# Kernel tuning notes

Measured on AMD Instinct MI355X. Metric: run time of the kernel, lower is better.

Reference implementation:

```python
import jax, jax.numpy as jnp
import numpy as np

H1, H2, H3 = 128, 64, 32   # hidden sizes from source constants
NT = 2                      # n_targets (P_I_meas, Q_I_meas)
NF = 16                     # n_features
B, T, S = 4096, 200, 20     # batch, history length, OUTPUT_STEPS


def setup_inputs() -> dict:
    key = jax.random.key(0)
    ks = jax.random.split(key, 16)
    s1 = 1.0 / np.sqrt(H1)  # pytorch LSTM init scale
    s2 = 1.0 / np.sqrt(H2)
    s3 = 1.0 / np.sqrt(H3)
    f32 = jnp.float32
    return {
        "x_history": jax.random.normal(ks[0], (B, T, NF), dtype=f32),
        "x_future_refs": jax.random.normal(ks[1], (B, S, NF - NT), dtype=f32),
        "Wih1": jax.random.normal(ks[2], (4 * H1, NF), dtype=f32) * s1,
        "Whh1": jax.random.normal(ks[3], (4 * H1, H1), dtype=f32) * s1,
        "bih1": jax.random.normal(ks[4], (4 * H1,), dtype=f32) * s1,
        "bhh1": jax.random.normal(ks[5], (4 * H1,), dtype=f32) * s1,
        "Wih2": jax.random.normal(ks[6], (4 * H2, H1), dtype=f32) * s2,
        "Whh2": jax.random.normal(ks[7], (4 * H2, H2), dtype=f32) * s2,
        "bih2": jax.random.normal(ks[8], (4 * H2,), dtype=f32) * s2,
        "bhh2": jax.random.normal(ks[9], (4 * H2,), dtype=f32) * s2,
        "Wd": jax.random.normal(ks[10], (H3, H2), dtype=f32) * s2,
        "bd": jax.random.normal(ks[11], (H3,), dtype=f32) * s2,
        "Wf": jax.random.normal(ks[12], (NT, H3), dtype=f32) * s3,
        "bf": jax.random.normal(ks[13], (NT,), dtype=f32) * s3,
        "out_bias": jnp.zeros((NT,), dtype=f32),
    }


def lstm_cell(x, h, c, Wih, Whh, bih, bhh):
    # PyTorch gate order: i, f, g, o
    g = x @ Wih.T + h @ Whh.T + (bih + bhh)
    i, f, gg, o = jnp.split(g, 4, axis=-1)
    c_new = jax.nn.sigmoid(f) * c + jax.nn.sigmoid(i) * jnp.tanh(gg)
    h_new = jax.nn.sigmoid(o) * jnp.tanh(c_new)
    return h_new, c_new


def reference(x_history, x_future_refs, Wih1, Whh1, bih1, bhh1,
              Wih2, Whh2, bih2, bhh2, Wd, bd, Wf, bf, out_bias):
    b = x_history.shape[0]
    dt = x_history.dtype
    h1 = jnp.zeros((b, H1), dt); c1 = jnp.zeros((b, H1), dt)
    h2 = jnp.zeros((b, H2), dt); c2 = jnp.zeros((b, H2), dt)

    # --- encode history: stacked 2-layer LSTM over T steps ---
    def enc_step(carry, xt):
        h1, c1, h2, c2 = carry
        h1, c1 = lstm_cell(xt, h1, c1, Wih1, Whh1, bih1, bhh1)
        h2, c2 = lstm_cell(h1, h2, c2, Wih2, Whh2, bih2, bhh2)
        return (h1, c1, h2, c2), None

    (h1, c1, h2, c2), _ = jax.lax.scan(
        enc_step, (h1, c1, h2, c2), jnp.swapaxes(x_history, 0, 1))

    # last history targets: x_history[:, -1, n_non_targets:]
    cur = x_history[:, -1, NF - NT:]

    def dec_step(carry, ref):
        h1, c1, h2, c2, cur = carry
        xin = jnp.concatenate([ref, cur], axis=1)  # [B, NF]
        h1, c1 = lstm_cell(xin, h1, c1, Wih1, Whh1, bih1, bhh1)
        h2, c2 = lstm_cell(h1, h2, c2, Wih2, Whh2, bih2, bhh2)
        d = jax.nn.relu(h2 @ Wd.T + bd)
        pred = d @ Wf.T + bf + out_bias
        return (h1, c1, h2, c2, pred), pred

    _, preds = jax.lax.scan(
        dec_step, (h1, c1, h2, c2, cur), jnp.swapaxes(x_future_refs, 0, 1))
    return jnp.swapaxes(preds, 0, 1)  # [B, S, NT]
```

## Files before the change

kernel.cpp:

```cpp
#include <hip/hip_runtime.h>

typedef unsigned short u16;
typedef unsigned int u32;

using short8 = __attribute__((ext_vector_type(8))) short;
using f32x4  = __attribute__((ext_vector_type(4))) float;

#define LOG2E 1.44269504088896340736f

#define X1S 168
#define H2S 72
#define DBS 40

__device__ __forceinline__ u16 f2bf(float f) {
  u32 u = __float_as_uint(f);
  return (u16)((u + 0x7FFFu + ((u >> 16) & 1u)) >> 16);
}
__device__ __forceinline__ float sigm(float x) {
  return __builtin_amdgcn_rcpf(1.0f + __builtin_amdgcn_exp2f(-LOG2E * x));
}
__device__ __forceinline__ float tanh_(float x) {
  return 1.0f - 2.0f * __builtin_amdgcn_rcpf(1.0f + __builtin_amdgcn_exp2f(2.0f * LOG2E * x));
}
__device__ __forceinline__ f32x4 mfma_(short8 a, short8 b, f32x4 c) {
  return __builtin_amdgcn_mfma_f32_16x16x32_bf16(a, b, c, 0, 0, 0);
}

__global__ __launch_bounds__(512, 1) void spc_lstm(
    const float* __restrict__ xh,   const float* __restrict__ xfr,
    const float* __restrict__ Wih1, const float* __restrict__ Whh1,
    const float* __restrict__ bih1, const float* __restrict__ bhh1,
    const float* __restrict__ Wih2, const float* __restrict__ Whh2,
    const float* __restrict__ bih2, const float* __restrict__ bhh2,
    const float* __restrict__ Wd,   const float* __restrict__ bd,
    const float* __restrict__ Wf,   const float* __restrict__ bfv,
    const float* __restrict__ ob,   float* __restrict__ out)
{
  __shared__ __align__(16) u16 X1[2][16 * X1S];
  __shared__ __align__(16) u16 H2B[2][16 * H2S];
  __shared__ __align__(16) u16 DB[16 * DBS];
  __shared__ __align__(16) u16 W1xF[32 * 256];
  __shared__ __align__(16) u16 W2F[64 * 512];
  __shared__ __align__(16) u16 WdF[4 * 512];
  __shared__ __align__(16) u16 WfF[512];
  __shared__ u16 PREDV[16][2];

  const int tid = threadIdx.x;
  const int wv  = tid >> 6;
  const int l   = tid & 63;
  const int c   = l & 15;
  const int q   = l >> 4;
  const int bb  = blockIdx.x << 4;
  const bool isA = (wv < 4);

  short8 w1h[4][4];
  short8 w2h[4][2];
  float  b1r[4];
  float  b2r[4] = {0.f, 0.f, 0.f, 0.f};

  for (int i = tid; i < 2 * 16 * X1S; i += 512) ((u16*)X1)[i] = 0;
  for (int i = tid; i < 2 * 16 * H2S; i += 512) ((u16*)H2B)[i] = 0;
  for (int i = tid; i < 16 * DBS; i += 512) DB[i] = 0;
  if (tid < 32) ((u16*)PREDV)[tid] = 0;
  __syncthreads();

  for (int i = tid; i < 64 * 512; i += 512) {
    const int rid = i >> 9, e = i & 511, k = e >> 4, n = e & 15;
    const int ww = rid >> 4, ty = (rid >> 2) & 3, kc = rid & 3;
    const int g = ty * 64 + ww * 16 + n;
    W2F[rid * 512 + ((k >> 3) * 16 + n) * 8 + (k & 7)] = f2bf(Wih2[g * 128 + kc * 32 + k]);
  }
  for (int i = tid; i < 32 * 256; i += 512) {
    const int T = i >> 8, e = i & 255, k = e >> 4, n = e & 15;
    const int ty = T >> 3, uv = T & 7;
    const int g = ty * 128 + uv * 16 + n;
    W1xF[T * 256 + ((k >> 3) * 16 + n) * 8 + (k & 7)] = f2bf(Wih1[g * 16 + k]);
  }
  for (int i = tid; i < 4 * 512; i += 512) {
    const int tix = i >> 9, e = i & 511, k = e >> 4, n = e & 15;
    const int ww = tix >> 1, kc2 = tix & 1;
    WdF[tix * 512 + ((k >> 3) * 16 + n) * 8 + (k & 7)] =
        f2bf(Wd[(ww * 16 + n) * 64 + kc2 * 32 + k]);
  }
  {
    const int k = tid >> 4, n = tid & 15;
    if (tid < 512)
      WfF[((k >> 3) * 16 + n) * 8 + (k & 7)] = (n < 2) ? f2bf(Wf[n * 32 + k]) : (u16)0;
  }

  #pragma unroll
  for (int ty = 0; ty < 4; ty++) {
    const int g = ty * 128 + wv * 16 + c;
    b1r[ty] = bih1[g] + bhh1[g];
    #pragma unroll
    for (int kc = 0; kc < 4; kc++) {
      short8 v;
      #pragma unroll
      for (int j = 0; j < 8; j++)
        v[j] = (short)f2bf(Whh1[g * 128 + kc * 32 + q * 8 + j]);
      w1h[ty][kc] = v;
    }
  }
  if (isA) {
    #pragma unroll
    for (int ty = 0; ty < 4; ty++) {
      const int g2 = ty * 64 + wv * 16 + c;
      b2r[ty] = bih2[g2] + bhh2[g2];
      #pragma unroll
      for (int kc = 0; kc < 2; kc++) {
        short8 v;
        #pragma unroll
        for (int j = 0; j < 8; j++)
          v[j] = (short)f2bf(Whh2[g2 * 64 + kc * 32 + q * 8 + j]);
        w2h[ty][kc] = v;
      }
    }
  }
  const float bdr = (wv == 4 || wv == 5) ? bd[(wv - 4) * 16 + c] : 0.f;
  const float bfr = (wv == 4 && c < 2) ? (bfv[c] + ob[c]) : 0.f;

  const int xi = tid - 256, xr = (xi >> 4) & 15, xcc = xi & 15;
  float xreg = 0.f; bool dreg = false;
  if (!isA) {
    X1[0][xr * X1S + 128 + xcc] = f2bf(xh[(bb + xr) * 3200 + xcc]);
    xreg = xh[(bb + xr) * 3200 + 16 + xcc]; dreg = true;
  }
  f32x4 c1 = (f32x4){0,0,0,0};
  f32x4 c2 = (f32x4){0,0,0,0};
  __syncthreads();

  for (int t = 0; t <= 220; t++) {
    u16* Xc    = X1[t & 1];
    u16* Xn    = X1[(t + 1) & 1];
    u16* Hprev = H2B[t & 1];
    u16* Hdst  = H2B[(t + 1) & 1];
    const bool dec  = (t >= 201);
    const bool doL1 = (t <= 219);
    const bool doL2 = isA && (t >= 1);

    if (doL2) {
      f32x4 acc2[4];
      #pragma unroll
      for (int ty = 0; ty < 4; ty++)
        acc2[ty] = (f32x4){b2r[ty], b2r[ty], b2r[ty], b2r[ty]};
      #pragma unroll
      for (int kc = 0; kc < 4; kc++) {
        const short8 fhi = *(const short8*)&Xc[c * X1S + kc * 32 + q * 8];
        #pragma unroll
        for (int ty = 0; ty < 4; ty++) {
          const short8 wf_ = *(const short8*)&W2F[(wv * 16 + ty * 4 + kc) * 512 + l * 8];
          acc2[ty] = mfma_(fhi, wf_, acc2[ty]);
        }
      }
      #pragma unroll
      for (int kc = 0; kc < 2; kc++) {
        const short8 hhi = *(const short8*)&Hprev[c * H2S + kc * 32 + q * 8];
        #pragma unroll
        for (int ty = 0; ty < 4; ty++)
          acc2[ty] = mfma_(hhi, w2h[ty][kc], acc2[ty]);
      }
      const int u = wv * 16 + c;
      #pragma unroll
      for (int r = 0; r < 4; r++) {
        float ig = sigm(acc2[0][r]);
        float fg = sigm(acc2[1][r]);
        float gg = tanh_(acc2[2][r]);
        float og = sigm(acc2[3][r]);
        float cn = fg * c2[r] + ig * gg;
        float hn = og * tanh_(cn);
        c2[r] = cn;
        Hdst[(q * 4 + r) * H2S + u] = f2bf(hn);
      }
    }

    if (!isA) {
      const float xw = xreg; const bool dw = dreg;
      const int s2 = t + 2;
      dreg = false;
      if (s2 < 200) { xreg = xh[(bb + xr) * 3200 + s2 * 16 + xcc]; dreg = true; }
      else if (s2 < 220) {
        const int s = s2 - 200;
        if (xcc < 14)    { xreg = xfr[(bb + xr) * 280 + s * 14 + xcc]; dreg = true; }
        else if (s == 0) { xreg = xh[(bb + xr) * 3200 + 199 * 16 + xcc]; dreg = true; }
      }
      if (dw) Xn[xr * X1S + 128 + xcc] = f2bf(xw);
    }

    if (dec) {
      __syncthreads();
      if (wv == 4 || wv == 5) {
        const int ww = wv - 4;
        f32x4 accd = (f32x4){bdr, bdr, bdr, bdr};
        #pragma unroll
        for (int kc = 0; kc < 2; kc++) {
          const short8 ad  = *(const short8*)&Hdst[c * H2S + kc * 32 + q * 8];
          const short8 wdk = *(const short8*)&WdF[(ww * 2 + kc) * 512 + l * 8];
          accd = mfma_(ad, wdk, accd);
        }
        #pragma unroll
        for (int r = 0; r < 4; r++)
          DB[(q * 4 + r) * DBS + ww * 16 + c] = f2bf(fmaxf(accd[r], 0.f));
      }
      __syncthreads();
      if (wv == 4) {
        const short8 ap  = *(const short8*)&DB[c * DBS + q * 8];
        const short8 wfv = *(const short8*)&WfF[l * 8];
        f32x4 accp = (f32x4){bfr, bfr, bfr, bfr};
        accp = mfma_(ap, wfv, accp);
        if (c < 2) {
          #pragma unroll
          for (int r = 0; r < 4; r++) {
            const int b = q * 4 + r;
            out[(bb + b) * 40 + (t - 201) * 2 + c] = accp[r];
            PREDV[b][c] = f2bf(accp[r]);
          }
        }
      }
      __syncthreads();
    }

    if (doL1) {
      f32x4 acc1[4];
      #pragma unroll
      for (int ty = 0; ty < 4; ty++)
        acc1[ty] = (f32x4){b1r[ty], b1r[ty], b1r[ty], b1r[ty]};
      #pragma unroll
      for (int kc = 0; kc < 4; kc++) {
        const short8 ahi = *(const short8*)&Xc[c * X1S + kc * 32 + q * 8];
        #pragma unroll
        for (int ty = 0; ty < 4; ty++)
          acc1[ty] = mfma_(ahi, w1h[ty][kc], acc1[ty]);
      }
      {
        short8 ax = *(const short8*)&Xc[c * X1S + 128 + q * 8];
        if (dec && q == 1) {
          ax[6] = (short)PREDV[c][0];
          ax[7] = (short)PREDV[c][1];
        }
        #pragma unroll
        for (int ty = 0; ty < 4; ty++) {
          short8 wxv = (short8){0,0,0,0,0,0,0,0};
          if (q < 2)
            wxv = *(const short8*)&W1xF[(ty * 8 + wv) * 256 + l * 8];
          acc1[ty] = mfma_(ax, wxv, acc1[ty]);
        }
      }
      const int u = wv * 16 + c;
      #pragma unroll
      for (int r = 0; r < 4; r++) {
        float ig = sigm(acc1[0][r]);
        float fg = sigm(acc1[1][r]);
        float gg = tanh_(acc1[2][r]);
        float og = sigm(acc1[3][r]);
        float cn = fg * c1[r] + ig * gg;
        float hn = og * tanh_(cn);
        c1[r] = cn;
        Xn[(q * 4 + r) * X1S + u] = f2bf(hn);
      }
    }
    __syncthreads();
  }
}

extern "C" void kernel_launch(void* const* d_in, const int* in_sizes, int n_in,
                              void* d_out, int out_size, void* d_ws, size_t ws_size,
                              hipStream_t stream) {
  (void)in_sizes; (void)n_in; (void)out_size; (void)d_ws; (void)ws_size;
  spc_lstm<<<dim3(256), dim3(512), 0, stream>>>(
      (const float*)d_in[0],  (const float*)d_in[1],
      (const float*)d_in[2],  (const float*)d_in[3],
      (const float*)d_in[4],  (const float*)d_in[5],
      (const float*)d_in[6],  (const float*)d_in[7],
      (const float*)d_in[8],  (const float*)d_in[9],
      (const float*)d_in[10], (const float*)d_in[11],
      (const float*)d_in[12], (const float*)d_in[13],
      (const float*)d_in[14], (float*)d_out);
}
```

Measured before the change: 468.9 us.

## Stage input features in 8-step chunks in LDS instead of per-step register prefetch

The per-step scalar global loads of the input features by waves 4-7 are replaced with vectorized float4 loads that fill an 8-timestep chunk buffer in LDS, double-buffered across chunks. The layer-1 input MFMA now reads its operand straight from that chunk buffer. Predictions are written back into the chunk slot, which removes the PREDV patching and the q<2 branch. The padded W1x layout grows to zero-filled 32-wide K, and X1's row stride shrinks. The aim is fewer small global loads and less per-step branching, at the cost of more LDS and periodic burst loads that may cause some waves to stall.

```diff
diff --git a/kernel.cpp b/kernel.cpp
--- a/kernel.cpp
+++ b/kernel.cpp
@@ -5,12 +5,14 @@
 
 using short8 = __attribute__((ext_vector_type(8))) short;
 using f32x4  = __attribute__((ext_vector_type(4))) float;
+using float4v = __attribute__((ext_vector_type(4))) float;
 
 #define LOG2E 1.44269504088896340736f
 
-#define X1S 168
+#define X1S 136
 #define H2S 72
 #define DBS 40
+#define XCS 328
 
 __device__ __forceinline__ u16 f2bf(float f) {
   u32 u = __float_as_uint(f);
@@ -39,11 +41,11 @@
   __shared__ __align__(16) u16 X1[2][16 * X1S];
   __shared__ __align__(16) u16 H2B[2][16 * H2S];
   __shared__ __align__(16) u16 DB[16 * DBS];
-  __shared__ __align__(16) u16 W1xF[32 * 256];
+  __shared__ __align__(16) u16 W1xF[32 * 512];
   __shared__ __align__(16) u16 W2F[64 * 512];
   __shared__ __align__(16) u16 WdF[4 * 512];
   __shared__ __align__(16) u16 WfF[512];
-  __shared__ u16 PREDV[16][2];
+  __shared__ __align__(16) u16 XCH[2][16 * XCS];
 
   const int tid = threadIdx.x;
   const int wv  = tid >> 6;
@@ -61,7 +63,7 @@
   for (int i = tid; i < 2 * 16 * X1S; i += 512) ((u16*)X1)[i] = 0;
   for (int i = tid; i < 2 * 16 * H2S; i += 512) ((u16*)H2B)[i] = 0;
   for (int i = tid; i < 16 * DBS; i += 512) DB[i] = 0;
-  if (tid < 32) ((u16*)PREDV)[tid] = 0;
+  for (int i = tid; i < 2 * 16 * XCS; i += 512) ((u16*)XCH)[i] = 0;
   __syncthreads();
 
   for (int i = tid; i < 64 * 512; i += 512) {
@@ -70,11 +72,12 @@
     const int g = ty * 64 + ww * 16 + n;
     W2F[rid * 512 + ((k >> 3) * 16 + n) * 8 + (k & 7)] = f2bf(Wih2[g * 128 + kc * 32 + k]);
   }
-  for (int i = tid; i < 32 * 256; i += 512) {
-    const int T = i >> 8, e = i & 255, k = e >> 4, n = e & 15;
+  for (int i = tid; i < 32 * 512; i += 512) {
+    const int T = i >> 9, e = i & 511, k = e >> 4, n = e & 15;
     const int ty = T >> 3, uv = T & 7;
     const int g = ty * 128 + uv * 16 + n;
-    W1xF[T * 256 + ((k >> 3) * 16 + n) * 8 + (k & 7)] = f2bf(Wih1[g * 16 + k]);
+    W1xF[T * 512 + ((k >> 3) * 16 + n) * 8 + (k & 7)] =
+        (k < 16) ? f2bf(Wih1[g * 16 + k]) : (u16)0;
   }
   for (int i = tid; i < 4 * 512; i += 512) {
     const int tix = i >> 9, e = i & 511, k = e >> 4, n = e & 15;
@@ -86,6 +89,18 @@
     const int k = tid >> 4, n = tid & 15;
     if (tid < 512)
       WfF[((k >> 3) * 16 + n) * 8 + (k & 7)] = (n < 2) ? f2bf(Wf[n * 32 + k]) : (u16)0;
+  }
+
+  if (!isA) {
+    const int i0 = tid - 256;
+    #pragma unroll
+    for (int p = 0; p < 2; p++) {
+      const int idx = i0 + p * 256;
+      const int r = idx >> 5, rem = idx & 31, st = rem >> 2, hf = rem & 3;
+      const float4v v = *(const float4v*)&xh[(bb + r) * 3200 + st * 16 + hf * 4];
+      u16* d = &XCH[0][r * XCS + st * 40 + hf * 4];
+      d[0] = f2bf(v[0]); d[1] = f2bf(v[1]); d[2] = f2bf(v[2]); d[3] = f2bf(v[3]);
+    }
   }
 
   #pragma unroll
@@ -119,12 +134,6 @@
   const float bdr = (wv == 4 || wv == 5) ? bd[(wv - 4) * 16 + c] : 0.f;
   const float bfr = (wv == 4 && c < 2) ? (bfv[c] + ob[c]) : 0.f;
 
-  const int xi = tid - 256, xr = (xi >> 4) & 15, xcc = xi & 15;
-  float xreg = 0.f; bool dreg = false;
-  if (!isA) {
-    X1[0][xr * X1S + 128 + xcc] = f2bf(xh[(bb + xr) * 3200 + xcc]);
-    xreg = xh[(bb + xr) * 3200 + 16 + xcc]; dreg = true;
-  }
   f32x4 c1 = (f32x4){0,0,0,0};
   f32x4 c2 = (f32x4){0,0,0,0};
   __syncthreads();
@@ -137,6 +146,39 @@
     const bool dec  = (t >= 201);
     const bool doL1 = (t <= 219);
     const bool doL2 = isA && (t >= 1);
+
+    if (!isA && (t & 7) == 0) {
+      const int cm = (t >> 3) + 1;
+      if (cm <= 27) {
+        u16* dst = XCH[cm & 1];
+        const int t0 = cm << 3;
+        if (cm <= 24) {
+          const int i0 = tid - 256;
+          #pragma unroll
+          for (int p = 0; p < 2; p++) {
+            const int idx = i0 + p * 256;
+            const int r = idx >> 5, rem = idx & 31, st = rem >> 2, hf = rem & 3;
+            const float4v v = *(const float4v*)&xh[(bb + r) * 3200 + (t0 + st) * 16 + hf * 4];
+            u16* d = &dst[r * XCS + st * 40 + hf * 4];
+            d[0] = f2bf(v[0]); d[1] = f2bf(v[1]); d[2] = f2bf(v[2]); d[3] = f2bf(v[3]);
+          }
+        } else {
+          for (int e = tid - 256; e < 16 * 8 * 14; e += 256) {
+            const int r = e / 112, rem2 = e % 112, st = rem2 / 14, f = rem2 % 14;
+            const int s8 = t0 + st;
+            if (s8 < 220)
+              dst[r * XCS + st * 40 + f] = f2bf(xfr[(bb + r) * 280 + (s8 - 200) * 14 + f]);
+          }
+          if (cm == 25) {
+            const int e = tid - 256;
+            if (e < 32) {
+              const int r = e >> 1, f = 14 + (e & 1);
+              dst[r * XCS + f] = f2bf(xh[(bb + r) * 3200 + 199 * 16 + f]);
+            }
+          }
+        }
+      }
+    }
 
     if (doL2) {
       f32x4 acc2[4];
@@ -173,19 +215,6 @@
       }
     }
 
-    if (!isA) {
-      const float xw = xreg; const bool dw = dreg;
-      const int s2 = t + 2;
-      dreg = false;
-      if (s2 < 200) { xreg = xh[(bb + xr) * 3200 + s2 * 16 + xcc]; dreg = true; }
-      else if (s2 < 220) {
-        const int s = s2 - 200;
-        if (xcc < 14)    { xreg = xfr[(bb + xr) * 280 + s * 14 + xcc]; dreg = true; }
-        else if (s == 0) { xreg = xh[(bb + xr) * 3200 + 199 * 16 + xcc]; dreg = true; }
-      }
-      if (dw) Xn[xr * X1S + 128 + xcc] = f2bf(xw);
-    }
-
     if (dec) {
       __syncthreads();
       if (wv == 4 || wv == 5) {
@@ -208,11 +237,12 @@
         f32x4 accp = (f32x4){bfr, bfr, bfr, bfr};
         accp = mfma_(ap, wfv, accp);
         if (c < 2) {
+          u16* slot = &XCH[(t >> 3) & 1][0];
           #pragma unroll
           for (int r = 0; r < 4; r++) {
             const int b = q * 4 + r;
             out[(bb + b) * 40 + (t - 201) * 2 + c] = accp[r];
-            PREDV[b][c] = f2bf(accp[r]);
+            slot[b * XCS + (t & 7) * 40 + 14 + c] = f2bf(accp[r]);
           }
         }
       }
@@ -232,16 +262,11 @@
           acc1[ty] = mfma_(ahi, w1h[ty][kc], acc1[ty]);
       }
       {
-        short8 ax = *(const short8*)&Xc[c * X1S + 128 + q * 8];
-        if (dec && q == 1) {
-          ax[6] = (short)PREDV[c][0];
-          ax[7] = (short)PREDV[c][1];
-        }
+        const short8 ax =
+            *(const short8*)&XCH[(t >> 3) & 1][c * XCS + (t & 7) * 40 + q * 8];
         #pragma unroll
         for (int ty = 0; ty < 4; ty++) {
-          short8 wxv = (short8){0,0,0,0,0,0,0,0};
-          if (q < 2)
-            wxv = *(const short8*)&W1xF[(ty * 8 + wv) * 256 + l * 8];
+          const short8 wxv = *(const short8*)&W1xF[(ty * 8 + wv) * 512 + l * 8];
           acc1[ty] = mfma_(ax, wxv, acc1[ty]);
         }
       }
```

New measurement: 459.9 us. Within noise of the previous version (-1.9%).
